# Optimization experiments

Measured on AMD Instinct MI355X. Metric: run time of the kernel, lower is better.

Reference implementation:

```python
import jax, jax.numpy as jnp
import numpy as np

C = 768; NUM_HEADS = 12; HID = 3072
HP = 14; WP = 14; TF = 8; BATCH = 4
EPS = 1e-5


def layer_norm(x, g, b):
    mu = jnp.mean(x, axis=-1, keepdims=True)
    var = jnp.mean((x - mu) ** 2, axis=-1, keepdims=True)
    return (x - mu) / jnp.sqrt(var + EPS) * g + b


def mha(x, qkv_w, qkv_b, proj_w, proj_b):
    # Manual multi-head softmax attention, faithful to Attention.forward.
    B, N, Cd = x.shape
    D = Cd // NUM_HEADS
    qkv = (x @ qkv_w.T + qkv_b).reshape(B, N, 3, NUM_HEADS, D).transpose(2, 0, 3, 1, 4)
    q, k, v = qkv[0], qkv[1], qkv[2]  # [B, H, N, D]
    attn = jax.nn.softmax(jnp.einsum('bhnd,bhmd->bhnm', q, k) * (D ** -0.5), axis=-1)
    out = jnp.einsum('bhnm,bhmd->bhnd', attn, v).transpose(0, 2, 1, 3).reshape(B, N, Cd)
    return out @ proj_w.T + proj_b


def setup_inputs() -> dict:
    key = jax.random.key(0)
    ks = jax.random.split(key, 16)
    p = lambda i, s: jax.random.normal(ks[i], s, jnp.float32) * 0.02
    N = 1 + HP * WP * TF  # cls token + spatial*temporal tokens
    return {
        'x': jax.random.normal(ks[0], (BATCH, N, C), jnp.float32),
        'ln_t_g': jnp.ones((C,), jnp.float32), 'ln_t_b': jnp.zeros((C,), jnp.float32),
        't_qkv_w': p(1, (3 * C, C)), 't_qkv_b': p(2, (3 * C,)),
        't_proj_w': p(3, (C, C)), 't_proj_b': p(4, (C,)),
        't_fc_w': p(5, (C, C)), 't_fc_b': p(6, (C,)),
        'ln1_g': jnp.ones((C,), jnp.float32), 'ln1_b': jnp.zeros((C,), jnp.float32),
        's_qkv_w': p(7, (3 * C, C)), 's_qkv_b': p(8, (3 * C,)),
        's_proj_w': p(9, (C, C)), 's_proj_b': p(10, (C,)),
        'ln2_g': jnp.ones((C,), jnp.float32), 'ln2_b': jnp.zeros((C,), jnp.float32),
        'fc1_w': p(11, (HID, C)), 'fc1_b': p(12, (HID,)),
        'fc2_w': p(13, (C, HID)), 'fc2_b': p(14, (C,)),
        'B': BATCH, 'T': TF, 'W': WP,
    }


def reference(x, ln_t_g, ln_t_b, t_qkv_w, t_qkv_b, t_proj_w, t_proj_b, t_fc_w, t_fc_b,
              ln1_g, ln1_b, s_qkv_w, s_qkv_b, s_proj_w, s_proj_b,
              ln2_g, ln2_b, fc1_w, fc1_b, fc2_w, fc2_b, B, T, W):
    # Block.forward, attention_type='divided_space_time', extra_tokens=0, is_cls=True.
    Bv, Ntot, Cd = x.shape
    H = ((Ntot - 1) // T) // W
    # --- temporal attention: 'b (h w t) m -> (b h w) t m' ---
    xt = x[:, 1:, :].reshape(B, H, W, T, Cd).reshape(B * H * W, T, Cd)
    res_t = mha(layer_norm(xt, ln_t_g, ln_t_b), t_qkv_w, t_qkv_b, t_proj_w, t_proj_b)
    res_t = res_t.reshape(B, H * W * T, Cd) @ t_fc_w.T + t_fc_b
    xt = x[:, 1:, :] + res_t  # [B, H*W*T, C]
    # --- spatial attention: 'b (h w t) m -> (b t) (h w) m' with cls token per frame ---
    init_cls = x[:, :1, :]  # [B, 1, C]
    cls_tok = jnp.repeat(init_cls, T, axis=1).reshape(B * T, 1, Cd)
    xs = xt.reshape(B, H, W, T, Cd).transpose(0, 3, 1, 2, 4).reshape(B * T, H * W, Cd)
    xs = jnp.concatenate([cls_tok, xs], axis=1)  # [(B*T), 1+H*W, C]
    res_s = mha(layer_norm(xs, ln1_g, ln1_b), s_qkv_w, s_qkv_b, s_proj_w, s_proj_b)
    cls_out = jnp.mean(res_s[:, 0, :].reshape(B, T, Cd), axis=1, keepdims=True)  # mean over frames
    res_s = res_s[:, 1:, :].reshape(B, T, H, W, Cd).transpose(0, 2, 3, 1, 4).reshape(B, H * W * T, Cd)
    x = jnp.concatenate([init_cls, xt], axis=1) + jnp.concatenate([cls_out, res_s], axis=1)
    # --- MLP (exact GELU, as nn.GELU default) ---
    h = layer_norm(x, ln2_g, ln2_b)
    h = jax.nn.gelu(h @ fc1_w.T + fc1_b, approximate=False)
    return x + (h @ fc2_w.T + fc2_b)
```

## Files before the change

### kernel.cpp

```cpp
#include <hip/hip_runtime.h>
#include <hip/hip_bf16.h>

typedef __bf16 bf16x8 __attribute__((ext_vector_type(8)));
typedef float f32x4 __attribute__((ext_vector_type(4)));
typedef __hip_bfloat16 bf16;

#define NTOK 1569

__device__ __forceinline__ void gl_lds16(const void* g, void* l) {
  __builtin_amdgcn_global_load_lds(
      (const __attribute__((address_space(1))) void*)g,
      (__attribute__((address_space(3))) void*)l, 16, 0, 0);
}

__global__ void cvt_bf16_k(const float* __restrict__ src, bf16* __restrict__ dst, int n) {
  int i = blockIdx.x * 256 + threadIdx.x;
  if (i < n) dst[i] = __float2bfloat16(src[i]);
}

__global__ void cvt_t_k(const float* __restrict__ src, bf16* __restrict__ dst) {
  int idx = blockIdx.x * 256 + threadIdx.x;
  int r = idx / 768, c = idx % 768;
  dst[(size_t)c * 768 + r] = __float2bfloat16(src[idx]);
}

__global__ __launch_bounds__(256) void bcomb_k(const float* __restrict__ Wf,
                                               const float* __restrict__ bp,
                                               const float* __restrict__ bfv,
                                               float* __restrict__ out) {
  int j = blockIdx.x * 4 + (threadIdx.x >> 6);
  int l = threadIdx.x & 63;
  if (j >= 768) return;
  float s = 0.f;
#pragma unroll
  for (int u = 0; u < 12; ++u) s += Wf[(size_t)j * 768 + l + 64 * u] * bp[l + 64 * u];
#pragma unroll
  for (int o = 1; o < 64; o <<= 1) s += __shfl_xor(s, o);
  if (l == 0) out[j] = s + bfv[j];
}

__global__ __launch_bounds__(256) void ln_k(
    const float* __restrict__ xsrc, const float* __restrict__ xt,
    const float* __restrict__ gam, const float* __restrict__ bet,
    bf16* __restrict__ y, int M, int mode) {
  int r = blockIdx.x * 4 + (threadIdx.x >> 6);
  int l = threadIdx.x & 63;
  if (r >= M) return;
  const float* src;
  if (mode == 0) {
    src = xsrc + (size_t)(r + r / 1568 + 1) * 768;
  } else if (mode == 1) {
    int g = r / 197, j = r % 197;
    int b = g >> 3, t = g & 7;
    if (j == 0) src = xsrc + (size_t)b * NTOK * 768;
    else        src = xt + (size_t)(b * 1568 + (j - 1) * 8 + t) * 768;
  } else {
    src = xsrc + (size_t)r * 768;
  }
  float vals[12], s = 0.f, s2 = 0.f;
#pragma unroll
  for (int u = 0; u < 12; ++u) {
    float v = src[l + 64 * u];
    vals[u] = v; s += v; s2 += v * v;
  }
#pragma unroll
  for (int o = 1; o < 64; o <<= 1) { s += __shfl_xor(s, o); s2 += __shfl_xor(s2, o); }
  float mu = s * (1.f / 768.f);
  float rstd = rsqrtf(s2 * (1.f / 768.f) - mu * mu + 1e-5f);
  bf16* yr = y + (size_t)r * 768;
#pragma unroll
  for (int u = 0; u < 12; ++u) {
    int c = l + 64 * u;
    yr[c] = __float2bfloat16((vals[u] - mu) * rstd * gam[c] + bet[c]);
  }
}

template <int BM, int BN, int WM, int WN, int OUTBF16, int RES, int GELU>
__global__ __launch_bounds__(WM * WN * 64, 2) void gemm_k(
    const bf16* __restrict__ X, const bf16* __restrict__ W,
    const float* __restrict__ bias, const float* __restrict__ resid,
    void* __restrict__ outp, int M, int N, int K) {
  constexpr int TH = WM * WN * 64;
  constexpr int MR = BM / (WM * 16);
  constexpr int NR = BN / (WN * 16);
  constexpr int CA = (BM * 64) / (TH * 16);
  constexpr int CB = (BN * 64) / (TH * 16);
  constexpr int BUFB = (BM + BN) * 64;
  __shared__ __align__(16) char LDS[4 * BUFB];
  const int tid = threadIdx.x;
  const int w = tid >> 6, l = tid & 63;
  const int wr = w / WN, wc = w % WN;
  const int lr = l & 15, lg = l >> 4;

  const int nwg = gridDim.x;
  const int orig = blockIdx.x;
  const int qd = nwg >> 3, rm = nwg & 7;
  const int xcd = orig & 7, lot = orig >> 3;
  const int swz = (xcd < rm ? xcd * (qd + 1) : rm * (qd + 1) + (xcd - rm) * qd) + lot;
  const int ntx = N / BN;
  const int m0 = (swz / ntx) * BM, n0 = (swz % ntx) * BN;

  const char* pA[CA]; const char* pB[CB]; int dA[CA], dB[CB];
#pragma unroll
  for (int i = 0; i < CA; ++i) {
    int d = (i * TH + w * 64 + l) * 16;
    int s = d ^ (((d >> 7) & 3) << 4);
    int r = s >> 6, cb = s & 63;
    int ga = m0 + r; if (ga >= M) ga = M - 1;
    pA[i] = (const char*)X + (size_t)ga * K * 2 + cb;
    dA[i] = d;
  }
#pragma unroll
  for (int i = 0; i < CB; ++i) {
    int d = (i * TH + w * 64 + l) * 16;
    int s = d ^ (((d >> 7) & 3) << 4);
    pB[i] = (const char*)W + (size_t)(n0 + (s >> 6)) * K * 2 + (s & 63);
    dB[i] = d;
  }

  auto stage = [&](int t, int buf) {
    char* Ab = LDS + buf * BUFB;
    char* Bb = Ab + BM * 64;
    size_t ko = (size_t)t * 64;
#pragma unroll
    for (int i = 0; i < CA; ++i) gl_lds16(pA[i] + ko, Ab + dA[i]);
#pragma unroll
    for (int i = 0; i < CB; ++i) gl_lds16(pB[i] + ko, Bb + dB[i]);
  };

  f32x4 acc[MR][NR] = {};
  const int nt = K >> 5;
  stage(0, 0);
  if (nt > 1) stage(1, 1);
  if (nt > 2) stage(2, 2);
  for (int t = 0; t < nt; ++t) {
    if (t + 3 < nt) {
      stage(t + 3, (t + 3) & 3);
      asm volatile("s_waitcnt vmcnt(12)" ::: "memory");
    } else if (t + 2 < nt) {
      asm volatile("s_waitcnt vmcnt(8)" ::: "memory");
    } else if (t + 1 < nt) {
      asm volatile("s_waitcnt vmcnt(4)" ::: "memory");
    } else {
      asm volatile("s_waitcnt vmcnt(0)" ::: "memory");
    }
    asm volatile("s_barrier" ::: "memory");
    const char* Ab = LDS + (t & 3) * BUFB;
    const char* Bb = Ab + BM * 64;
    bf16x8 af[MR], bg[NR];
#pragma unroll
    for (int mf = 0; mf < MR; ++mf) {
      int row = wr * (MR * 16) + mf * 16 + lr;
      int d = row * 64 + lg * 16;
      af[mf] = *(const bf16x8*)(Ab + (d ^ (((d >> 7) & 3) << 4)));
    }
#pragma unroll
    for (int nf = 0; nf < NR; ++nf) {
      int row = wc * (NR * 16) + nf * 16 + lr;
      int d = row * 64 + lg * 16;
      bg[nf] = *(const bf16x8*)(Bb + (d ^ (((d >> 7) & 3) << 4)));
    }
    __builtin_amdgcn_s_setprio(1);
#pragma unroll
    for (int mf = 0; mf < MR; ++mf)
#pragma unroll
      for (int nf = 0; nf < NR; ++nf)
        acc[mf][nf] = __builtin_amdgcn_mfma_f32_16x16x32_bf16(af[mf], bg[nf], acc[mf][nf], 0, 0, 0);
    __builtin_amdgcn_s_setprio(0);
    asm volatile("s_barrier" ::: "memory");
  }

  const float* bp = bias; const float* rp = resid;
  asm volatile("" : "+s"(bp), "+s"(rp));
#pragma unroll
  for (int mf = 0; mf < MR; ++mf) {
    int rowb = m0 + wr * (MR * 16) + mf * 16 + lg * 4;
#pragma unroll
    for (int nf = 0; nf < NR; ++nf) {
      int col = n0 + wc * (NR * 16) + nf * 16 + lr;
      float bv = bp ? bp[col] : 0.f;
#pragma unroll
      for (int q = 0; q < 4; ++q) {
        int row = rowb + q;
        if (row < M) {
          float v = acc[mf][nf][q] + bv;
          if (GELU) v = 0.5f * v * (1.f + erff(v * 0.70710678118654752f));
          if (RES == 1) v += rp[(size_t)(row + row / 1568 + 1) * 768 + col];
          if (RES == 2) v += rp[(size_t)row * N + col];
          if (OUTBF16) ((bf16*)outp)[(size_t)row * N + col] = __float2bfloat16(v);
          else         ((float*)outp)[(size_t)row * N + col] = v;
        }
      }
    }
  }
}

__global__ __launch_bounds__(256) void attn_t_k(const bf16* __restrict__ qkv,
                                                bf16* __restrict__ outp) {
  __shared__ float sh[4][3 * 520];
  const int wv = threadIdx.x >> 6, l = threadIdx.x & 63;
  const int g = blockIdx.x * 4 + wv;
  const int sq = g / 12, hd = g % 12;
  float* qs = sh[wv];
  float* ks = qs + 520;
  float* vs = qs + 1040;
  const bf16* base = qkv + (size_t)sq * 8 * 2304 + hd * 64;
#pragma unroll
  for (int i = 0; i < 8; ++i) {
    const bf16* rp = base + (size_t)i * 2304;
    qs[i * 65 + l] = __bfloat162float(rp[l]);
    ks[i * 65 + l] = __bfloat162float(rp[768 + l]);
    vs[i * 65 + l] = __bfloat162float(rp[1536 + l]);
  }
  __builtin_amdgcn_wave_barrier();
  const int i = l >> 3, j = l & 7;
  float s = 0.f;
#pragma unroll
  for (int d = 0; d < 64; ++d) s += qs[i * 65 + d] * ks[j * 65 + d];
  s *= 0.125f;
  float m = s;
  m = fmaxf(m, __shfl_xor(m, 1));
  m = fmaxf(m, __shfl_xor(m, 2));
  m = fmaxf(m, __shfl_xor(m, 4));
  float p = __expf(s - m);
  float sum = p;
  sum += __shfl_xor(sum, 1);
  sum += __shfl_xor(sum, 2);
  sum += __shfl_xor(sum, 4);
  p /= sum;
  float pr[8];
#pragma unroll
  for (int jj = 0; jj < 8; ++jj) pr[jj] = __shfl(p, i * 8 + jj);
  bf16* op = outp + (size_t)(sq * 8) * 768 + hd * 64;
#pragma unroll
  for (int u = 0; u < 8; ++u) {
    int c = j + 8 * u;
    float o = 0.f;
#pragma unroll
    for (int jj = 0; jj < 8; ++jj) o += pr[jj] * vs[jj * 65 + c];
    op[(size_t)i * 768 + c] = __float2bfloat16(o);
  }
}

__global__ __launch_bounds__(256) void build_vt_k(const bf16* __restrict__ qkv,
                                                  bf16* __restrict__ vt) {
  const int sq = blockIdx.x / 12, hd = blockIdx.x % 12;
  const bf16* vsrc = qkv + (size_t)sq * 197 * 2304 + 1536 + hd * 64;
  bf16* dst = vt + (size_t)blockIdx.x * 64 * 224;
  for (int idx = threadIdx.x; idx < 197 * 64; idx += 256) {
    int j = idx >> 6, d = idx & 63;
    dst[d * 224 + j] = vsrc[(size_t)j * 2304 + d];
  }
}

__global__ __launch_bounds__(256) void attn_s_k(
    const bf16* __restrict__ qkv, const bf16* __restrict__ vt,
    bf16* __restrict__ outp) {
  __shared__ __align__(16) bf16 P[4][16 * 232];
  const int wv = threadIdx.x >> 6, l = threadIdx.x & 63;
  const int sq = blockIdx.x / 12, hd = blockIdx.x % 12;
  const int lr = l & 15, lg = l >> 4;
  bf16* Pw = P[wv];
#pragma unroll
  for (int idx = 0; idx < 4; ++idx) {
    int e = idx * 64 + l;
    Pw[(e >> 4) * 232 + 208 + (e & 15)] = __float2bfloat16(0.f);
  }
  const bf16* qbase = qkv + (size_t)sq * 197 * 2304 + hd * 64;
  const bf16* kbase = qbase + 768;
  const bf16* vbase = vt + (size_t)blockIdx.x * 64 * 224;
  for (int qt = wv; qt < 13; qt += 4) {
    int q0 = qt * 16;
    int qrow = q0 + lr; if (qrow > 196) qrow = 196;
    bf16x8 qa0 = *(const bf16x8*)(qbase + (size_t)qrow * 2304 + lg * 8);
    bf16x8 qa1 = *(const bf16x8*)(qbase + (size_t)qrow * 2304 + 32 + lg * 8);
    f32x4 sacc[13];
#pragma unroll
    for (int jt = 0; jt < 13; ++jt) {
      const bf16* kp = kbase + (size_t)(jt * 16 + lr) * 2304;
      bf16x8 kb0 = *(const bf16x8*)(kp + lg * 8);
      bf16x8 kb1 = *(const bf16x8*)(kp + 32 + lg * 8);
      f32x4 z = {};
      z = __builtin_amdgcn_mfma_f32_16x16x32_bf16(qa0, kb0, z, 0, 0, 0);
      z = __builtin_amdgcn_mfma_f32_16x16x32_bf16(qa1, kb1, z, 0, 0, 0);
      sacc[jt] = z;
    }
#pragma unroll
    for (int jt = 0; jt < 13; ++jt) {
      bool valid = (jt * 16 + lr) < 197;
#pragma unroll
      for (int q = 0; q < 4; ++q)
        sacc[jt][q] = valid ? sacc[jt][q] * 0.125f : -3e38f;
    }
    float inv[4];
#pragma unroll
    for (int q = 0; q < 4; ++q) {
      float m = -3e38f;
#pragma unroll
      for (int jt = 0; jt < 13; ++jt) m = fmaxf(m, sacc[jt][q]);
      m = fmaxf(m, __shfl_xor(m, 1));
      m = fmaxf(m, __shfl_xor(m, 2));
      m = fmaxf(m, __shfl_xor(m, 4));
      m = fmaxf(m, __shfl_xor(m, 8));
      float ssum = 0.f;
#pragma unroll
      for (int jt = 0; jt < 13; ++jt) {
        float p = __expf(sacc[jt][q] - m);
        sacc[jt][q] = p;
        ssum += p;
      }
      ssum += __shfl_xor(ssum, 1);
      ssum += __shfl_xor(ssum, 2);
      ssum += __shfl_xor(ssum, 4);
      ssum += __shfl_xor(ssum, 8);
      inv[q] = 1.f / ssum;
    }
#pragma unroll
    for (int jt = 0; jt < 13; ++jt)
#pragma unroll
      for (int q = 0; q < 4; ++q)
        Pw[(lg * 4 + q) * 232 + jt * 16 + lr] = __float2bfloat16(sacc[jt][q]);
    __builtin_amdgcn_wave_barrier();
    f32x4 oacc[4] = {};
#pragma unroll
    for (int j7 = 0; j7 < 7; ++j7) {
      bf16x8 pa = *(const bf16x8*)(Pw + lr * 232 + j7 * 32 + lg * 8);
#pragma unroll
      for (int n = 0; n < 4; ++n) {
        bf16x8 vb = *(const bf16x8*)(vbase + (size_t)(n * 16 + lr) * 224 + j7 * 32 + lg * 8);
        oacc[n] = __builtin_amdgcn_mfma_f32_16x16x32_bf16(pa, vb, oacc[n], 0, 0, 0);
      }
    }
    __builtin_amdgcn_wave_barrier();
#pragma unroll
    for (int n = 0; n < 4; ++n)
#pragma unroll
      for (int q = 0; q < 4; ++q) {
        int orow = q0 + lg * 4 + q;
        if (orow < 197)
          outp[(size_t)(sq * 197 + orow) * 768 + hd * 64 + n * 16 + lr] =
              __float2bfloat16(oacc[n][q] * inv[q]);
      }
  }
}

__global__ __launch_bounds__(256) void combine_k(
    const float* __restrict__ x, const float* __restrict__ xt,
    const float* __restrict__ rs, float* __restrict__ xn) {
  int r = blockIdx.x;
  int b = r / NTOK, n = r % NTOK;
  for (int c = threadIdx.x; c < 768; c += 256) {
    float v;
    if (n == 0) {
      float a = 0.f;
#pragma unroll
      for (int t = 0; t < 8; ++t) a += rs[(size_t)((b * 8 + t) * 197) * 768 + c];
      v = x[(size_t)r * 768 + c] + a * 0.125f;
    } else {
      int hw = (n - 1) >> 3, t = (n - 1) & 7;
      v = xt[(size_t)(b * 1568 + n - 1) * 768 + c] +
          rs[(size_t)((b * 8 + t) * 197 + 1 + hw) * 768 + c];
    }
    xn[(size_t)r * 768 + c] = v;
  }
}

extern "C" void kernel_launch(void* const* d_in, const int* in_sizes, int n_in,
                              void* d_out, int out_size, void* d_ws, size_t ws_size,
                              hipStream_t stream) {
  (void)in_sizes; (void)n_in; (void)out_size; (void)ws_size;
  const float* x        = (const float*)d_in[0];
  const float* ln_t_g   = (const float*)d_in[1];
  const float* ln_t_b   = (const float*)d_in[2];
  const float* t_qkv_w  = (const float*)d_in[3];
  const float* t_qkv_b  = (const float*)d_in[4];
  const float* t_proj_w = (const float*)d_in[5];
  const float* t_proj_b = (const float*)d_in[6];
  const float* t_fc_w   = (const float*)d_in[7];
  const float* t_fc_b   = (const float*)d_in[8];
  const float* ln1_g    = (const float*)d_in[9];
  const float* ln1_b    = (const float*)d_in[10];
  const float* s_qkv_w  = (const float*)d_in[11];
  const float* s_qkv_b  = (const float*)d_in[12];
  const float* s_proj_w = (const float*)d_in[13];
  const float* s_proj_b = (const float*)d_in[14];
  const float* ln2_g    = (const float*)d_in[15];
  const float* ln2_b    = (const float*)d_in[16];
  const float* fc1_w    = (const float*)d_in[17];
  const float* fc1_b    = (const float*)d_in[18];
  const float* fc2_w    = (const float*)d_in[19];
  const float* fc2_b    = (const float*)d_in[20];

  char* ws = (char*)d_ws;
  size_t o = 0;
  auto alloc = [&](size_t bytes) { size_t r = o; o += (bytes + 255) & ~(size_t)255; return r; };
  bf16* wqkvt  = (bf16*)(ws + alloc((size_t)2304 * 768 * 2));
  bf16* wqkvs  = (bf16*)(ws + alloc((size_t)2304 * 768 * 2));
  bf16* wprojs = (bf16*)(ws + alloc((size_t)768 * 768 * 2));
  bf16* wfct   = (bf16*)(ws + alloc((size_t)768 * 768 * 2));
  bf16* wpT    = (bf16*)(ws + alloc((size_t)768 * 768 * 2));
  bf16* wcomb  = (bf16*)(ws + alloc((size_t)768 * 768 * 2));
  float* bcomb = (float*)(ws + alloc((size_t)768 * 4));
  bf16* wfc1   = (bf16*)(ws + alloc((size_t)3072 * 768 * 2));
  bf16* wfc2   = (bf16*)(ws + alloc((size_t)768 * 3072 * 2));
  bf16* ybuf   = (bf16*)(ws + alloc((size_t)6400 * 768 * 2));
  char* big    = ws + alloc((size_t)6400 * 3072 * 2);
  bf16* qkvb   = (bf16*)big;
  bf16* h1     = (bf16*)big;
  bf16* abuf   = (bf16*)(ws + alloc((size_t)6400 * 768 * 2));
  char* slotS  = ws + alloc((size_t)6304 * 768 * 4);
  bf16* vtb    = (bf16*)slotS;
  float* rsb   = (float*)slotS;
  float* xtb   = (float*)(ws + alloc((size_t)6272 * 768 * 4));
  float* xnb   = (float*)(ws + alloc((size_t)6276 * 768 * 4));

  cvt_bf16_k<<<(2304 * 768 + 255) / 256, 256, 0, stream>>>(t_qkv_w, wqkvt, 2304 * 768);
  cvt_bf16_k<<<(2304 * 768 + 255) / 256, 256, 0, stream>>>(s_qkv_w, wqkvs, 2304 * 768);
  cvt_bf16_k<<<(768 * 768 + 255) / 256, 256, 0, stream>>>(s_proj_w, wprojs, 768 * 768);
  cvt_bf16_k<<<(768 * 768 + 255) / 256, 256, 0, stream>>>(t_fc_w, wfct, 768 * 768);
  cvt_t_k<<<2304, 256, 0, stream>>>(t_proj_w, wpT);
  cvt_bf16_k<<<(3072 * 768 + 255) / 256, 256, 0, stream>>>(fc1_w, wfc1, 3072 * 768);
  cvt_bf16_k<<<(3072 * 768 + 255) / 256, 256, 0, stream>>>(fc2_w, wfc2, 3072 * 768);
  bcomb_k<<<192, 256, 0, stream>>>(t_fc_w, t_proj_b, t_fc_b, bcomb);
  gemm_k<128, 128, 2, 2, 1, 0, 0><<<36, 256, 0, stream>>>(wfct, wpT, nullptr, nullptr, wcomb, 768, 768, 768);

  ln_k<<<1568, 256, 0, stream>>>(x, nullptr, ln_t_g, ln_t_b, ybuf, 6272, 0);
  gemm_k<256, 256, 2, 4, 1, 0, 0><<<225, 512, 0, stream>>>(ybuf, wqkvt, t_qkv_b, nullptr, qkvb, 6272, 2304, 768);
  attn_t_k<<<2352, 256, 0, stream>>>(qkvb, abuf);
  gemm_k<128, 128, 2, 2, 0, 1, 0><<<294, 256, 0, stream>>>(abuf, wcomb, bcomb, x, xtb, 6272, 768, 768);

  ln_k<<<1576, 256, 0, stream>>>(x, xtb, ln1_g, ln1_b, ybuf, 6304, 1);
  gemm_k<256, 256, 2, 4, 1, 0, 0><<<225, 512, 0, stream>>>(ybuf, wqkvs, s_qkv_b, nullptr, qkvb, 6304, 2304, 768);
  build_vt_k<<<384, 256, 0, stream>>>(qkvb, vtb);
  attn_s_k<<<384, 256, 0, stream>>>(qkvb, vtb, abuf);
  gemm_k<128, 128, 2, 2, 0, 0, 0><<<300, 256, 0, stream>>>(abuf, wprojs, s_proj_b, nullptr, rsb, 6304, 768, 768);

  combine_k<<<6276, 256, 0, stream>>>(x, xtb, rsb, xnb);

  ln_k<<<1569, 256, 0, stream>>>(xnb, nullptr, ln2_g, ln2_b, ybuf, 6276, 2);
  gemm_k<256, 256, 2, 4, 1, 0, 1><<<300, 512, 0, stream>>>(ybuf, wfc1, fc1_b, nullptr, h1, 6276, 3072, 768);
  gemm_k<128, 128, 2, 2, 0, 2, 0><<<300, 256, 0, stream>>>(h1, wfc2, fc2_b, xnb, (float*)d_out, 6276, 768, 3072);
}
```

Baseline: 609.7 us.

## Fuse combine with LayerNorm, vectorize conversions, unify GEMM to 128x128 tiles

Fuses the residual combine and the final LayerNorm into one kernel, removing a full fp32 round trip of the combined activations. LayerNorm and the weight conversions now use float4 loads and packed bf16 stores. The GEMM template is fixed to 128x128 tiles with 256 threads, three LDS buffers and three blocks per CU. The large 256x256 GEMMs (QKV, fc1) now use this smaller tile, giving more workgroups and occupancy but less data reuse per tile.

Result: faster. 564.8 us (-7.4%).

```diff
diff --git a/kernel.cpp b/kernel.cpp
--- a/kernel.cpp
+++ b/kernel.cpp
@@ -13,9 +13,21 @@
       (__attribute__((address_space(3))) void*)l, 16, 0, 0);
 }
 
-__global__ void cvt_bf16_k(const float* __restrict__ src, bf16* __restrict__ dst, int n) {
+__device__ __forceinline__ unsigned short bf16bits(float v) {
+  union { __hip_bfloat16 h; unsigned short u; } cv;
+  cv.h = __float2bfloat16(v);
+  return cv.u;
+}
+
+__global__ void cvt_bf16_k(const float4* __restrict__ src, uint2* __restrict__ dst, int n4) {
   int i = blockIdx.x * 256 + threadIdx.x;
-  if (i < n) dst[i] = __float2bfloat16(src[i]);
+  if (i < n4) {
+    float4 v = src[i];
+    union { unsigned short h[4]; uint2 u; } pk;
+    pk.h[0] = bf16bits(v.x); pk.h[1] = bf16bits(v.y);
+    pk.h[2] = bf16bits(v.z); pk.h[3] = bf16bits(v.w);
+    dst[i] = pk.u;
+  }
 }
 
 __global__ void cvt_t_k(const float* __restrict__ src, bf16* __restrict__ dst) {
@@ -49,47 +61,113 @@
   const float* src;
   if (mode == 0) {
     src = xsrc + (size_t)(r + r / 1568 + 1) * 768;
-  } else if (mode == 1) {
+  } else {
     int g = r / 197, j = r % 197;
     int b = g >> 3, t = g & 7;
     if (j == 0) src = xsrc + (size_t)b * NTOK * 768;
     else        src = xt + (size_t)(b * 1568 + (j - 1) * 8 + t) * 768;
-  } else {
-    src = xsrc + (size_t)r * 768;
-  }
-  float vals[12], s = 0.f, s2 = 0.f;
-#pragma unroll
-  for (int u = 0; u < 12; ++u) {
-    float v = src[l + 64 * u];
-    vals[u] = v; s += v; s2 += v * v;
+  }
+  const float4* s4 = (const float4*)src;
+  const float4* g4 = (const float4*)gam;
+  const float4* b4 = (const float4*)bet;
+  float4 v[3]; float s = 0.f, s2 = 0.f;
+#pragma unroll
+  for (int u = 0; u < 3; ++u) {
+    float4 t4 = s4[l + 64 * u];
+    v[u] = t4;
+    s += t4.x + t4.y + t4.z + t4.w;
+    s2 += t4.x * t4.x + t4.y * t4.y + t4.z * t4.z + t4.w * t4.w;
   }
 #pragma unroll
   for (int o = 1; o < 64; o <<= 1) { s += __shfl_xor(s, o); s2 += __shfl_xor(s2, o); }
   float mu = s * (1.f / 768.f);
   float rstd = rsqrtf(s2 * (1.f / 768.f) - mu * mu + 1e-5f);
-  bf16* yr = y + (size_t)r * 768;
-#pragma unroll
-  for (int u = 0; u < 12; ++u) {
-    int c = l + 64 * u;
-    yr[c] = __float2bfloat16((vals[u] - mu) * rstd * gam[c] + bet[c]);
-  }
-}
-
-template <int BM, int BN, int WM, int WN, int OUTBF16, int RES, int GELU>
-__global__ __launch_bounds__(WM * WN * 64, 2) void gemm_k(
+  uint2* yr = (uint2*)(y + (size_t)r * 768);
+#pragma unroll
+  for (int u = 0; u < 3; ++u) {
+    int j = l + 64 * u;
+    float4 gg = g4[j], bb = b4[j];
+    union { unsigned short h[4]; uint2 u2; } pk;
+    pk.h[0] = bf16bits((v[u].x - mu) * rstd * gg.x + bb.x);
+    pk.h[1] = bf16bits((v[u].y - mu) * rstd * gg.y + bb.y);
+    pk.h[2] = bf16bits((v[u].z - mu) * rstd * gg.z + bb.z);
+    pk.h[3] = bf16bits((v[u].w - mu) * rstd * gg.w + bb.w);
+    yr[j] = pk.u2;
+  }
+}
+
+__global__ __launch_bounds__(256) void combine_ln_k(
+    const float* __restrict__ x, const float* __restrict__ xt,
+    const float* __restrict__ rs, const float* __restrict__ gam,
+    const float* __restrict__ bet, float* __restrict__ xn,
+    bf16* __restrict__ y) {
+  int r = blockIdx.x * 4 + (threadIdx.x >> 6);
+  int l = threadIdx.x & 63;
+  if (r >= 4 * NTOK) return;
+  int b = r / NTOK, n = r % NTOK;
+  float4 v[3]; float s = 0.f, s2 = 0.f;
+  if (n == 0) {
+#pragma unroll
+    for (int u = 0; u < 3; ++u) {
+      int j = l + 64 * u;
+      float4 a = {0.f, 0.f, 0.f, 0.f};
+#pragma unroll
+      for (int t = 0; t < 8; ++t) {
+        float4 rv = ((const float4*)(rs + (size_t)((b * 8 + t) * 197) * 768))[j];
+        a.x += rv.x; a.y += rv.y; a.z += rv.z; a.w += rv.w;
+      }
+      float4 xv = ((const float4*)(x + (size_t)r * 768))[j];
+      v[u].x = xv.x + a.x * 0.125f; v[u].y = xv.y + a.y * 0.125f;
+      v[u].z = xv.z + a.z * 0.125f; v[u].w = xv.w + a.w * 0.125f;
+    }
+  } else {
+    int hw = (n - 1) >> 3, t = (n - 1) & 7;
+    const float4* xt4 = (const float4*)(xt + (size_t)(b * 1568 + n - 1) * 768);
+    const float4* rs4 = (const float4*)(rs + (size_t)((b * 8 + t) * 197 + 1 + hw) * 768);
+#pragma unroll
+    for (int u = 0; u < 3; ++u) {
+      int j = l + 64 * u;
+      float4 a = xt4[j], c = rs4[j];
+      v[u].x = a.x + c.x; v[u].y = a.y + c.y; v[u].z = a.z + c.z; v[u].w = a.w + c.w;
+    }
+  }
+  float4* xn4 = (float4*)(xn + (size_t)r * 768);
+#pragma unroll
+  for (int u = 0; u < 3; ++u) {
+    xn4[l + 64 * u] = v[u];
+    s += v[u].x + v[u].y + v[u].z + v[u].w;
+    s2 += v[u].x * v[u].x + v[u].y * v[u].y + v[u].z * v[u].z + v[u].w * v[u].w;
+  }
+#pragma unroll
+  for (int o = 1; o < 64; o <<= 1) { s += __shfl_xor(s, o); s2 += __shfl_xor(s2, o); }
+  float mu = s * (1.f / 768.f);
+  float rstd = rsqrtf(s2 * (1.f / 768.f) - mu * mu + 1e-5f);
+  const float4* g4 = (const float4*)gam;
+  const float4* b4 = (const float4*)bet;
+  uint2* yr = (uint2*)(y + (size_t)r * 768);
+#pragma unroll
+  for (int u = 0; u < 3; ++u) {
+    int j = l + 64 * u;
+    float4 gg = g4[j], bb = b4[j];
+    union { unsigned short h[4]; uint2 u2; } pk;
+    pk.h[0] = bf16bits((v[u].x - mu) * rstd * gg.x + bb.x);
+    pk.h[1] = bf16bits((v[u].y - mu) * rstd * gg.y + bb.y);
+    pk.h[2] = bf16bits((v[u].z - mu) * rstd * gg.z + bb.z);
+    pk.h[3] = bf16bits((v[u].w - mu) * rstd * gg.w + bb.w);
+    yr[j] = pk.u2;
+  }
+}
+
+template <int OUTBF16, int RES, int GELU>
+__global__ __launch_bounds__(256, 3) void gemm_k(
     const bf16* __restrict__ X, const bf16* __restrict__ W,
     const float* __restrict__ bias, const float* __restrict__ resid,
     void* __restrict__ outp, int M, int N, int K) {
-  constexpr int TH = WM * WN * 64;
-  constexpr int MR = BM / (WM * 16);
-  constexpr int NR = BN / (WN * 16);
-  constexpr int CA = (BM * 64) / (TH * 16);
-  constexpr int CB = (BN * 64) / (TH * 16);
-  constexpr int BUFB = (BM + BN) * 64;
-  __shared__ __align__(16) char LDS[4 * BUFB];
+  constexpr int BUFB = 256 * 64;
+  __shared__ __align__(16) char LDS[3 * BUFB];
   const int tid = threadIdx.x;
   const int w = tid >> 6, l = tid & 63;
-  const int wr = w / WN, wc = w % WN;
+  const int wr = w >> 1, wc = w & 1;
   const int lr = l & 15, lg = l >> 4;
 
   const int nwg = gridDim.x;
@@ -97,47 +175,41 @@
   const int qd = nwg >> 3, rm = nwg & 7;
   const int xcd = orig & 7, lot = orig >> 3;
   const int swz = (xcd < rm ? xcd * (qd + 1) : rm * (qd + 1) + (xcd - rm) * qd) + lot;
-  const int ntx = N / BN;
-  const int m0 = (swz / ntx) * BM, n0 = (swz % ntx) * BN;
-
-  const char* pA[CA]; const char* pB[CB]; int dA[CA], dB[CB];
-#pragma unroll
-  for (int i = 0; i < CA; ++i) {
-    int d = (i * TH + w * 64 + l) * 16;
+  const int ntx = N >> 7;
+  const int m0 = (swz / ntx) << 7, n0 = (swz % ntx) << 7;
+
+  const char* pA[2]; const char* pB[2]; int dA[2], dB[2];
+#pragma unroll
+  for (int i = 0; i < 2; ++i) {
+    int d = (i * 256 + tid) * 16;
     int s = d ^ (((d >> 7) & 3) << 4);
     int r = s >> 6, cb = s & 63;
     int ga = m0 + r; if (ga >= M) ga = M - 1;
     pA[i] = (const char*)X + (size_t)ga * K * 2 + cb;
-    dA[i] = d;
-  }
-#pragma unroll
-  for (int i = 0; i < CB; ++i) {
-    int d = (i * TH + w * 64 + l) * 16;
-    int s = d ^ (((d >> 7) & 3) << 4);
-    pB[i] = (const char*)W + (size_t)(n0 + (s >> 6)) * K * 2 + (s & 63);
-    dB[i] = d;
-  }
-
-  auto stage = [&](int t, int buf) {
+    pB[i] = (const char*)W + (size_t)(n0 + r) * K * 2 + (s & 63);
+    dA[i] = d; dB[i] = d;
+  }
+
+  auto stage = [&](size_t ko, int buf) {
     char* Ab = LDS + buf * BUFB;
-    char* Bb = Ab + BM * 64;
-    size_t ko = (size_t)t * 64;
-#pragma unroll
-    for (int i = 0; i < CA; ++i) gl_lds16(pA[i] + ko, Ab + dA[i]);
-#pragma unroll
-    for (int i = 0; i < CB; ++i) gl_lds16(pB[i] + ko, Bb + dB[i]);
+    char* Bb = Ab + 128 * 64;
+#pragma unroll
+    for (int i = 0; i < 2; ++i) gl_lds16(pA[i] + ko, Ab + dA[i]);
+#pragma unroll
+    for (int i = 0; i < 2; ++i) gl_lds16(pB[i] + ko, Bb + dB[i]);
   };
 
-  f32x4 acc[MR][NR] = {};
+  f32x4 acc[4][4] = {};
   const int nt = K >> 5;
   stage(0, 0);
-  if (nt > 1) stage(1, 1);
-  if (nt > 2) stage(2, 2);
+  stage(64, 1);
+  size_t ko2 = 128;
+  int bufS = 2, bufC = 0;
   for (int t = 0; t < nt; ++t) {
-    if (t + 3 < nt) {
-      stage(t + 3, (t + 3) & 3);
-      asm volatile("s_waitcnt vmcnt(12)" ::: "memory");
-    } else if (t + 2 < nt) {
+    if (t + 2 < nt) {
+      stage(ko2, bufS);
+      ko2 += 64;
+      bufS = (bufS == 2) ? 0 : bufS + 1;
       asm volatile("s_waitcnt vmcnt(8)" ::: "memory");
     } else if (t + 1 < nt) {
       asm volatile("s_waitcnt vmcnt(4)" ::: "memory");
@@ -145,48 +217,45 @@
       asm volatile("s_waitcnt vmcnt(0)" ::: "memory");
     }
     asm volatile("s_barrier" ::: "memory");
-    const char* Ab = LDS + (t & 3) * BUFB;
-    const char* Bb = Ab + BM * 64;
-    bf16x8 af[MR], bg[NR];
-#pragma unroll
-    for (int mf = 0; mf < MR; ++mf) {
-      int row = wr * (MR * 16) + mf * 16 + lr;
-      int d = row * 64 + lg * 16;
+    const char* Ab = LDS + bufC * BUFB;
+    const char* Bb = Ab + 128 * 64;
+    bufC = (bufC == 2) ? 0 : bufC + 1;
+    bf16x8 af[4], bg[4];
+#pragma unroll
+    for (int mf = 0; mf < 4; ++mf) {
+      int d = (wr * 64 + mf * 16 + lr) * 64 + lg * 16;
       af[mf] = *(const bf16x8*)(Ab + (d ^ (((d >> 7) & 3) << 4)));
     }
 #pragma unroll
-    for (int nf = 0; nf < NR; ++nf) {
-      int row = wc * (NR * 16) + nf * 16 + lr;
-      int d = row * 64 + lg * 16;
+    for (int nf = 0; nf < 4; ++nf) {
+      int d = (wc * 64 + nf * 16 + lr) * 64 + lg * 16;
       bg[nf] = *(const bf16x8*)(Bb + (d ^ (((d >> 7) & 3) << 4)));
     }
     __builtin_amdgcn_s_setprio(1);
 #pragma unroll
-    for (int mf = 0; mf < MR; ++mf)
-#pragma unroll
-      for (int nf = 0; nf < NR; ++nf)
+    for (int mf = 0; mf < 4; ++mf)
+#pragma unroll
+      for (int nf = 0; nf < 4; ++nf)
         acc[mf][nf] = __builtin_amdgcn_mfma_f32_16x16x32_bf16(af[mf], bg[nf], acc[mf][nf], 0, 0, 0);
     __builtin_amdgcn_s_setprio(0);
     asm volatile("s_barrier" ::: "memory");
   }
 
-  const float* bp = bias; const float* rp = resid;
-  asm volatile("" : "+s"(bp), "+s"(rp));
-#pragma unroll
-  for (int mf = 0; mf < MR; ++mf) {
-    int rowb = m0 + wr * (MR * 16) + mf * 16 + lg * 4;
-#pragma unroll
-    for (int nf = 0; nf < NR; ++nf) {
-      int col = n0 + wc * (NR * 16) + nf * 16 + lr;
-      float bv = bp ? bp[col] : 0.f;
+#pragma unroll
+  for (int mf = 0; mf < 4; ++mf) {
+    int rowb = m0 + wr * 64 + mf * 16 + lg * 4;
+#pragma unroll
+    for (int nf = 0; nf < 4; ++nf) {
+      int col = n0 + wc * 64 + nf * 16 + lr;
+      float bv = bias ? bias[col] : 0.f;
 #pragma unroll
       for (int q = 0; q < 4; ++q) {
         int row = rowb + q;
         if (row < M) {
           float v = acc[mf][nf][q] + bv;
           if (GELU) v = 0.5f * v * (1.f + erff(v * 0.70710678118654752f));
-          if (RES == 1) v += rp[(size_t)(row + row / 1568 + 1) * 768 + col];
-          if (RES == 2) v += rp[(size_t)row * N + col];
+          if (RES == 1) v += resid[(size_t)(row + row / 1568 + 1) * 768 + col];
+          if (RES == 2) v += resid[(size_t)row * N + col];
           if (OUTBF16) ((bf16*)outp)[(size_t)row * N + col] = __float2bfloat16(v);
           else         ((float*)outp)[(size_t)row * N + col] = v;
         }
@@ -341,27 +410,6 @@
           outp[(size_t)(sq * 197 + orow) * 768 + hd * 64 + n * 16 + lr] =
               __float2bfloat16(oacc[n][q] * inv[q]);
       }
-  }
-}
-
-__global__ __launch_bounds__(256) void combine_k(
-    const float* __restrict__ x, const float* __restrict__ xt,
-    const float* __restrict__ rs, float* __restrict__ xn) {
-  int r = blockIdx.x;
-  int b = r / NTOK, n = r % NTOK;
-  for (int c = threadIdx.x; c < 768; c += 256) {
-    float v;
-    if (n == 0) {
-      float a = 0.f;
-#pragma unroll
-      for (int t = 0; t < 8; ++t) a += rs[(size_t)((b * 8 + t) * 197) * 768 + c];
-      v = x[(size_t)r * 768 + c] + a * 0.125f;
-    } else {
-      int hw = (n - 1) >> 3, t = (n - 1) & 7;
-      v = xt[(size_t)(b * 1568 + n - 1) * 768 + c] +
-          rs[(size_t)((b * 8 + t) * 197 + 1 + hw) * 768 + c];
-    }
-    xn[(size_t)r * 768 + c] = v;
   }
 }
 
@@ -414,30 +462,29 @@
   float* xtb   = (float*)(ws + alloc((size_t)6272 * 768 * 4));
   float* xnb   = (float*)(ws + alloc((size_t)6276 * 768 * 4));
 
-  cvt_bf16_k<<<(2304 * 768 + 255) / 256, 256, 0, stream>>>(t_qkv_w, wqkvt, 2304 * 768);
-  cvt_bf16_k<<<(2304 * 768 + 255) / 256, 256, 0, stream>>>(s_qkv_w, wqkvs, 2304 * 768);
-  cvt_bf16_k<<<(768 * 768 + 255) / 256, 256, 0, stream>>>(s_proj_w, wprojs, 768 * 768);
-  cvt_bf16_k<<<(768 * 768 + 255) / 256, 256, 0, stream>>>(t_fc_w, wfct, 768 * 768);
+  cvt_bf16_k<<<1728, 256, 0, stream>>>((const float4*)t_qkv_w, (uint2*)wqkvt, 442368);
+  cvt_bf16_k<<<1728, 256, 0, stream>>>((const float4*)s_qkv_w, (uint2*)wqkvs, 442368);
+  cvt_bf16_k<<<576, 256, 0, stream>>>((const float4*)s_proj_w, (uint2*)wprojs, 147456);
+  cvt_bf16_k<<<576, 256, 0, stream>>>((const float4*)t_fc_w, (uint2*)wfct, 147456);
   cvt_t_k<<<2304, 256, 0, stream>>>(t_proj_w, wpT);
-  cvt_bf16_k<<<(3072 * 768 + 255) / 256, 256, 0, stream>>>(fc1_w, wfc1, 3072 * 768);
-  cvt_bf16_k<<<(3072 * 768 + 255) / 256, 256, 0, stream>>>(fc2_w, wfc2, 3072 * 768);
+  cvt_bf16_k<<<2304, 256, 0, stream>>>((const float4*)fc1_w, (uint2*)wfc1, 589824);
+  cvt_bf16_k<<<2304, 256, 0, stream>>>((const float4*)fc2_w, (uint2*)wfc2, 589824);
   bcomb_k<<<192, 256, 0, stream>>>(t_fc_w, t_proj_b, t_fc_b, bcomb);
-  gemm_k<128, 128, 2, 2, 1, 0, 0><<<36, 256, 0, stream>>>(wfct, wpT, nullptr, nullptr, wcomb, 768, 768, 768);
+  gemm_k<1, 0, 0><<<36, 256, 0, stream>>>(wfct, wpT, nullptr, nullptr, wcomb, 768, 768, 768);
 
   ln_k<<<1568, 256, 0, stream>>>(x, nullptr, ln_t_g, ln_t_b, ybuf, 6272, 0);
-  gemm_k<256, 256, 2, 4, 1, 0, 0><<<225, 512, 0, stream>>>(ybuf, wqkvt, t_qkv_b, nullptr, qkvb, 6272, 2304, 768);
+  gemm_k<1, 0, 0><<<882, 256, 0, stream>>>(ybuf, wqkvt, t_qkv_b, nullptr, qkvb, 6272, 2304, 768);
   attn_t_k<<<2352, 256, 0, stream>>>(qkvb, abuf);
-  gemm_k<128, 128, 2, 2, 0, 1, 0><<<294, 256, 0, stream>>>(abuf, wcomb, bcomb, x, xtb, 6272, 768, 768);
+  gemm_k<0, 1, 0><<<294, 256, 0, stream>>>(abuf, wcomb, bcomb, x, xtb, 6272, 768, 768);
 
   ln_k<<<1576, 256, 0, stream>>>(x, xtb, ln1_g, ln1_b, ybuf, 6304, 1);
-  gemm_k<256, 256, 2, 4, 1, 0, 0><<<225, 512, 0, stream>>>(ybuf, wqkvs, s_qkv_b, nullptr, qkvb, 6304, 2304, 768);
+  gemm_k<1, 0, 0><<<900, 256, 0, stream>>>(ybuf, wqkvs, s_qkv_b, nullptr, qkvb, 6304, 2304, 768);
   build_vt_k<<<384, 256, 0, stream>>>(qkvb, vtb);
   attn_s_k<<<384, 256, 0, stream>>>(qkvb, vtb, abuf);
-  gemm_k<128, 128, 2, 2, 0, 0, 0><<<300, 256, 0, stream>>>(abuf, wprojs, s_proj_b, nullptr, rsb, 6304, 768, 768);
-
-  combine_k<<<6276, 256, 0, stream>>>(x, xtb, rsb, xnb);
-
-  ln_k<<<1569, 256, 0, stream>>>(xnb, nullptr, ln2_g, ln2_b, ybuf, 6276, 2);
-  gemm_k<256, 256, 2, 4, 1, 0, 1><<<300, 512, 0, stream>>>(ybuf, wfc1, fc1_b, nullptr, h1, 6276, 3072, 768);
-  gemm_k<128, 128, 2, 2, 0, 2, 0><<<300, 256, 0, stream>>>(h1, wfc2, fc2_b, xnb, (float*)d_out, 6276, 768, 3072);
-}
+  gemm_k<0, 0, 0><<<300, 256, 0, stream>>>(abuf, wprojs, s_proj_b, nullptr, rsb, 6304, 768, 768);
+
+  combine_ln_k<<<1569, 256, 0, stream>>>(x, xtb, rsb, ln2_g, ln2_b, xnb, ybuf);
+
+  gemm_k<1, 0, 1><<<1200, 256, 0, stream>>>(ybuf, wfc1, fc1_b, nullptr, h1, 6276, 3072, 768);
+  gemm_k<0, 2, 0><<<300, 256, 0, stream>>>(h1, wfc2, fc2_b, xnb, (float*)d_out, 6276, 768, 3072);
+}
```
